# Optimization experiments

Hardware: AMD Instinct MI355X
Metric: run time of the kernel (lower is better)

## Reference

```python
import jax, jax.numpy as jnp
import numpy as np

C_CURV = 1.0          # manifold curvature c
MIN_NORM = 1e-15      # hgcn min-norm clamp
ATANH_EPS = 1e-6      # artanh arg clamp (fp32-safe version of hgcn's 1e-15)

N_NODES, DIM, N_EDGES, N_CLASSES = 100000, 128, 1000000, 4


def setup_inputs() -> dict:
    key = jax.random.key(0)
    k1, k2, k3 = jax.random.split(key, 3)
    x = jax.random.normal(k1, (N_NODES, DIM), dtype=jnp.float32)
    idx = jax.random.randint(k2, (N_EDGES, 2), 0, N_NODES, dtype=jnp.int64)
    W = jax.random.normal(k3, (2 * DIM, N_CLASSES), dtype=jnp.float32) * 0.05
    b = jnp.zeros((N_CLASSES,), dtype=jnp.float32)
    return {"x": x, "idx": idx, "W": W, "b": b}


def _logmap0(x, c):
    # PoincareBall.logmap0: scale = artanh(sqrt(c)*||x||) / (sqrt(c)*||x||)
    sqrt_c = c ** 0.5
    norm = jnp.maximum(jnp.linalg.norm(x, axis=-1, keepdims=True), MIN_NORM)
    a = jnp.clip(sqrt_c * norm, -1.0 + ATANH_EPS, 1.0 - ATANH_EPS)
    return (jnp.arctanh(a) / (sqrt_c * norm)) * x


def reference(x, idx, W, b):
    # proj_tan0 is identity for the Poincare ball
    h = _logmap0(x, C_CURV)                                   # [N, D]
    edge_feat = jnp.concatenate([h[idx[:, 0]], h[idx[:, 1]]], axis=1)  # [E, 2D]
    # Linear with identity activation (dropout=0 at inference)
    return edge_feat @ W + b                                  # [E, n_classes]
```

## Files before the change

kernel.cpp:

```cpp
#include <hip/hip_runtime.h>
#include <hip/hip_bf16.h>


#define DIM 128

typedef float f32x4 __attribute__((ext_vector_type(4)));
typedef int   i32x2 __attribute__((ext_vector_type(2)));

__global__ __launch_bounds__(256) void node_proj_kernel(
    const float* __restrict__ x, const float* __restrict__ W,
    const float* __restrict__ b, float* __restrict__ y, int n_nodes)
{
    __shared__ f32x4 xs[32 * 33];
    __shared__ float wp[1056];
    const int t = threadIdx.x;
    {
        const f32x4 wv = ((const f32x4*)W)[t];
        const int r = t & 127, h = t >> 7;
        *(f32x4*)(wp + r * 8 + (r >> 4) * 4 + h * 4) = wv;
    }

    const int gbase = blockIdx.x * 32;

    const f32x4* xg = (const f32x4*)x;
#pragma unroll
    for (int s = t; s < 1024; s += 256) {
        const int row = s >> 5, c4 = s & 31;
        const int gn = gbase + row;
        f32x4 v = {0.f, 0.f, 0.f, 0.f};
        if (gn < n_nodes) v = xg[(size_t)gn * 32 + c4];
        xs[row * 33 + c4] = v;
    }
    __syncthreads();

    const int lane = t & 63;
    const int li   = lane & 7;
    const int g    = lane >> 3;
    const int r    = (t >> 6) * 8 + g;
    const int n    = gbase + r;
    if (n >= n_nodes) return;

    const f32x4* xrow = &xs[r * 33 + li * 4];
    const float* wl   = wp + li * 132;

    f32x4 xa[4];
#pragma unroll
    for (int q = 0; q < 4; ++q) xa[q] = xrow[q];

    float acc[9];
#pragma unroll
    for (int i = 0; i < 9; ++i) acc[i] = 0.f;

#pragma unroll
    for (int q = 0; q < 4; ++q) {
#pragma unroll
        for (int k = 0; k < 4; ++k) {
            const int idx = q * 4 + k;
            const f32x4 wa = *(const f32x4*)(wl + idx * 8);
            const f32x4 wb = *(const f32x4*)(wl + idx * 8 + 4);
            const float a = xa[q][k];
            acc[0] = fmaf(a, a, acc[0]);
            acc[1] = fmaf(a, wa[0], acc[1]);
            acc[2] = fmaf(a, wa[1], acc[2]);
            acc[3] = fmaf(a, wa[2], acc[3]);
            acc[4] = fmaf(a, wa[3], acc[4]);
            acc[5] = fmaf(a, wb[0], acc[5]);
            acc[6] = fmaf(a, wb[1], acc[6]);
            acc[7] = fmaf(a, wb[2], acc[7]);
            acc[8] = fmaf(a, wb[3], acc[8]);
        }
    }

#pragma unroll
    for (int i = 0; i < 9; ++i) {
        acc[i] += __shfl_xor(acc[i], 1, 64);
        acc[i] += __shfl_xor(acc[i], 2, 64);
        acc[i] += __shfl_xor(acc[i], 4, 64);
    }

    if (li < 2) {
        const bool second = li;

        float norm = fmaxf(sqrtf(acc[0]), 1e-15f);
        const float aa  = fminf(norm, 1.0f - 1e-6f);
        const float art = 0.5f * log1pf(2.0f * aa / (1.0f - aa));
        const float scale = art / norm;

        const float w0 = second ? acc[5] : acc[1];
        const float w1 = second ? acc[6] : acc[2];
        const float w2 = second ? acc[7] : acc[3];
        const float w3 = second ? acc[8] : acc[4];

        const f32x4 bv4 = *(const f32x4*)b;
        f32x4 o;
        o[0] = fmaf(w0, scale, second ? 0.f : bv4[0]);
        o[1] = fmaf(w1, scale, second ? 0.f : bv4[1]);
        o[2] = fmaf(w2, scale, second ? 0.f : bv4[2]);
        o[3] = fmaf(w3, scale, second ? 0.f : bv4[3]);

        *(f32x4*)(y + (size_t)n * 8 + li * 4) = o;
    }
}

__global__ __launch_bounds__(256) void edge_kernel(
    const int* __restrict__ idx, const float* __restrict__ y,
    float* __restrict__ out, int n_edges)
{
    const int e = blockIdx.x * blockDim.x + threadIdx.x;
    if (e >= n_edges) return;
    const i32x2 ii = __builtin_nontemporal_load((const i32x2*)idx + e);
    const f32x4 a0 = *(const f32x4*)(y + (size_t)ii[0] * 8);
    const f32x4 c0 = *(const f32x4*)(y + (size_t)ii[1] * 8 + 4);
    const f32x4 o0 = a0 + c0;
    __builtin_nontemporal_store(o0, (f32x4*)out + e);
}

extern "C" void kernel_launch(void* const* d_in, const int* in_sizes, int n_in,
                              void* d_out, int out_size, void* d_ws, size_t ws_size,
                              hipStream_t stream) {
    const float* x   = (const float*)d_in[0];
    const int*   idx = (const int*)d_in[1];
    const float* W   = (const float*)d_in[2];
    const float* b   = (const float*)d_in[3];
    float* out = (float*)d_out;

    const int n_nodes = in_sizes[0] / DIM;
    const int n_edges = in_sizes[1] / 2;

    float* y = (float*)d_ws;

    const int blocks1 = (n_nodes + 31) / 32;
    node_proj_kernel<<<blocks1, 256, 0, stream>>>(x, W, b, y, n_nodes);

    const int blocks2 = (n_edges + 255) / 256;
    edge_kernel<<<blocks2, 256, 0, stream>>>(idx, y, out, n_edges);
}
```

Measured before the change: 34.42 us.

## Make node projection persistent with register-staged prefetch of next tile

The node projection kernel now runs a fixed grid of 1024 blocks that loop over 32-row tiles. Each block loads W into shared memory once, and while computing the current tile it prefetches the next tile's rows into registers, then copies them into shared memory between two barriers. Each thread now loads four contiguous float4s of one row instead of strided elements. The aim is to amortize the W setup and hide global load latency behind compute, at the cost of extra registers, two barriers per tile and fewer blocks in flight.

```diff
diff --git a/kernel.cpp b/kernel.cpp
--- a/kernel.cpp
+++ b/kernel.cpp
@@ -3,13 +3,15 @@
 
 
 #define DIM 128
+#define NODE_BLOCKS 1024
 
 typedef float f32x4 __attribute__((ext_vector_type(4)));
 typedef int   i32x2 __attribute__((ext_vector_type(2)));
 
 __global__ __launch_bounds__(256) void node_proj_kernel(
     const float* __restrict__ x, const float* __restrict__ W,
-    const float* __restrict__ b, float* __restrict__ y, int n_nodes)
+    const float* __restrict__ b, float* __restrict__ y,
+    int n_nodes, int ntiles)
 {
     __shared__ f32x4 xs[32 * 33];
     __shared__ float wp[1056];
@@ -20,16 +22,19 @@
         *(f32x4*)(wp + r * 8 + (r >> 4) * 4 + h * 4) = wv;
     }
 
-    const int gbase = blockIdx.x * 32;
+    const int srow = t >> 3;
+    const int sc4  = (t & 7) * 4;
+    const f32x4* xg = (const f32x4*)x;
 
-    const f32x4* xg = (const f32x4*)x;
+    int tile = blockIdx.x;
+    {
+        const int gn = tile * 32 + srow;
 #pragma unroll
-    for (int s = t; s < 1024; s += 256) {
-        const int row = s >> 5, c4 = s & 31;
-        const int gn = gbase + row;
-        f32x4 v = {0.f, 0.f, 0.f, 0.f};
-        if (gn < n_nodes) v = xg[(size_t)gn * 32 + c4];
-        xs[row * 33 + c4] = v;
+        for (int q = 0; q < 4; ++q) {
+            f32x4 v = {0.f, 0.f, 0.f, 0.f};
+            if (gn < n_nodes) v = xg[(size_t)gn * 32 + sc4 + q];
+            xs[srow * 33 + sc4 + q] = v;
+        }
     }
     __syncthreads();
 
@@ -37,68 +42,91 @@
     const int li   = lane & 7;
     const int g    = lane >> 3;
     const int r    = (t >> 6) * 8 + g;
-    const int n    = gbase + r;
-    if (n >= n_nodes) return;
+    const float* wl = wp + li * 132;
+    const f32x4 bv4 = *(const f32x4*)b;
 
-    const f32x4* xrow = &xs[r * 33 + li * 4];
-    const float* wl   = wp + li * 132;
+    for (; tile < ntiles; tile += NODE_BLOCKS) {
+        const int ntile = tile + NODE_BLOCKS;
 
-    f32x4 xa[4];
+        f32x4 stg[4];
+        const bool have_next = ntile < ntiles;
+        if (have_next) {
+            const int gn = ntile * 32 + srow;
 #pragma unroll
-    for (int q = 0; q < 4; ++q) xa[q] = xrow[q];
+            for (int q = 0; q < 4; ++q) {
+                f32x4 v = {0.f, 0.f, 0.f, 0.f};
+                if (gn < n_nodes) v = xg[(size_t)gn * 32 + sc4 + q];
+                stg[q] = v;
+            }
+        }
 
-    float acc[9];
+        const int n = tile * 32 + r;
+        if (n < n_nodes) {
+            const f32x4* xrow = &xs[r * 33 + li * 4];
+            f32x4 xa[4];
 #pragma unroll
-    for (int i = 0; i < 9; ++i) acc[i] = 0.f;
+            for (int q = 0; q < 4; ++q) xa[q] = xrow[q];
+
+            float acc[9];
+#pragma unroll
+            for (int i = 0; i < 9; ++i) acc[i] = 0.f;
 
 #pragma unroll
-    for (int q = 0; q < 4; ++q) {
+            for (int q = 0; q < 4; ++q) {
 #pragma unroll
-        for (int k = 0; k < 4; ++k) {
-            const int idx = q * 4 + k;
-            const f32x4 wa = *(const f32x4*)(wl + idx * 8);
-            const f32x4 wb = *(const f32x4*)(wl + idx * 8 + 4);
-            const float a = xa[q][k];
-            acc[0] = fmaf(a, a, acc[0]);
-            acc[1] = fmaf(a, wa[0], acc[1]);
-            acc[2] = fmaf(a, wa[1], acc[2]);
-            acc[3] = fmaf(a, wa[2], acc[3]);
-            acc[4] = fmaf(a, wa[3], acc[4]);
-            acc[5] = fmaf(a, wb[0], acc[5]);
-            acc[6] = fmaf(a, wb[1], acc[6]);
-            acc[7] = fmaf(a, wb[2], acc[7]);
-            acc[8] = fmaf(a, wb[3], acc[8]);
-        }
-    }
+                for (int k = 0; k < 4; ++k) {
+                    const int di = q * 4 + k;
+                    const f32x4 wa = *(const f32x4*)(wl + di * 8);
+                    const f32x4 wb = *(const f32x4*)(wl + di * 8 + 4);
+                    const float a = xa[q][k];
+                    acc[0] = fmaf(a, a, acc[0]);
+                    acc[1] = fmaf(a, wa[0], acc[1]);
+                    acc[2] = fmaf(a, wa[1], acc[2]);
+                    acc[3] = fmaf(a, wa[2], acc[3]);
+                    acc[4] = fmaf(a, wa[3], acc[4]);
+                    acc[5] = fmaf(a, wb[0], acc[5]);
+                    acc[6] = fmaf(a, wb[1], acc[6]);
+                    acc[7] = fmaf(a, wb[2], acc[7]);
+                    acc[8] = fmaf(a, wb[3], acc[8]);
+                }
+            }
 
 #pragma unroll
-    for (int i = 0; i < 9; ++i) {
-        acc[i] += __shfl_xor(acc[i], 1, 64);
-        acc[i] += __shfl_xor(acc[i], 2, 64);
-        acc[i] += __shfl_xor(acc[i], 4, 64);
-    }
+            for (int i = 0; i < 9; ++i) {
+                acc[i] += __shfl_xor(acc[i], 1, 64);
+                acc[i] += __shfl_xor(acc[i], 2, 64);
+                acc[i] += __shfl_xor(acc[i], 4, 64);
+            }
 
-    if (li < 2) {
-        const bool second = li;
+            if (li < 2) {
+                const bool second = li;
+                float norm = fmaxf(sqrtf(acc[0]), 1e-15f);
+                const float aa  = fminf(norm, 1.0f - 1e-6f);
+                const float art = 0.5f * log1pf(2.0f * aa / (1.0f - aa));
+                const float scale = art / norm;
 
-        float norm = fmaxf(sqrtf(acc[0]), 1e-15f);
-        const float aa  = fminf(norm, 1.0f - 1e-6f);
-        const float art = 0.5f * log1pf(2.0f * aa / (1.0f - aa));
-        const float scale = art / norm;
+                const float w0 = second ? acc[5] : acc[1];
+                const float w1 = second ? acc[6] : acc[2];
+                const float w2 = second ? acc[7] : acc[3];
+                const float w3 = second ? acc[8] : acc[4];
 
-        const float w0 = second ? acc[5] : acc[1];
-        const float w1 = second ? acc[6] : acc[2];
-        const float w2 = second ? acc[7] : acc[3];
-        const float w3 = second ? acc[8] : acc[4];
+                f32x4 o;
+                o[0] = fmaf(w0, scale, second ? 0.f : bv4[0]);
+                o[1] = fmaf(w1, scale, second ? 0.f : bv4[1]);
+                o[2] = fmaf(w2, scale, second ? 0.f : bv4[2]);
+                o[3] = fmaf(w3, scale, second ? 0.f : bv4[3]);
 
-        const f32x4 bv4 = *(const f32x4*)b;
-        f32x4 o;
-        o[0] = fmaf(w0, scale, second ? 0.f : bv4[0]);
-        o[1] = fmaf(w1, scale, second ? 0.f : bv4[1]);
-        o[2] = fmaf(w2, scale, second ? 0.f : bv4[2]);
-        o[3] = fmaf(w3, scale, second ? 0.f : bv4[3]);
+                *(f32x4*)(y + (size_t)n * 8 + li * 4) = o;
+            }
+        }
 
-        *(f32x4*)(y + (size_t)n * 8 + li * 4) = o;
+        if (have_next) {
+            __syncthreads();
+#pragma unroll
+            for (int q = 0; q < 4; ++q)
+                xs[srow * 33 + sc4 + q] = stg[q];
+            __syncthreads();
+        }
     }
 }
 
@@ -129,8 +157,9 @@
 
     float* y = (float*)d_ws;
 
-    const int blocks1 = (n_nodes + 31) / 32;
-    node_proj_kernel<<<blocks1, 256, 0, stream>>>(x, W, b, y, n_nodes);
+    const int ntiles = (n_nodes + 31) / 32;
+    node_proj_kernel<<<NODE_BLOCKS, 256, 0, stream>>>(x, W, b, y,
+                                                      n_nodes, ntiles);
 
     const int blocks2 = (n_edges + 255) / 256;
     edge_kernel<<<blocks2, 256, 0, stream>>>(idx, y, out, n_edges);
```

Result: slower. 36.22 us (+5.2%).
